# Kernel tuning notes

Measured on AMD Instinct MI355X. Metric: run time of the kernel, lower is better.

The kernel has to match this reference:

```python
import jax, jax.numpy as jnp
import numpy as np

B, S = 64, 100
N_EX, N_Q = 3000, 128
N_AT, N_IT = 1000, 1000
D_A = D_E = D_K = 128
GAMMA = 0.03


def _xavier(k, shape):
    lim = float(np.sqrt(6.0 / (shape[0] + shape[1])))
    return jax.random.uniform(k, shape, jnp.float32, -lim, lim)


def setup_inputs() -> dict:
    key = jax.random.key(0)
    ks = jax.random.split(key, 20)
    nq1 = N_Q + 1
    e_data = jax.random.randint(ks[0], (B, S), 0, N_EX, dtype=jnp.int32)
    a_data = jax.random.randint(ks[1], (B, S), 0, 2, dtype=jnp.int32)
    it_data = jax.random.randint(ks[2], (B, S), 0, N_IT, dtype=jnp.int32)
    at_data = jax.random.randint(ks[3], (B, S), 0, N_AT, dtype=jnp.int32)
    # binary Q-matrix with zeros replaced by gamma (as done in LPKT.__init__)
    q_bin = (jax.random.uniform(ks[4], (N_EX + 10, nq1)) < 0.05).astype(jnp.float32)
    q_matrix = jnp.where(q_bin > 0, 1.0, GAMMA)
    E_at = _xavier(ks[5], (N_AT + 10, D_K))
    E_it = _xavier(ks[6], (N_IT + 10, D_K))
    E_e = _xavier(ks[7], (N_EX + 10, D_E))
    h0 = _xavier(ks[8], (nq1, D_K))  # xavier-initialized initial skill state
    W1 = _xavier(ks[9], (D_A + D_E + D_K, D_K)); b1 = jnp.zeros(D_K, jnp.float32)
    W2 = _xavier(ks[10], (4 * D_K, D_K)); b2 = jnp.zeros(D_K, jnp.float32)
    W3 = _xavier(ks[11], (4 * D_K, D_K)); b3 = jnp.zeros(D_K, jnp.float32)
    W4 = _xavier(ks[12], (3 * D_K, D_K)); b4 = jnp.zeros(D_K, jnp.float32)
    W5 = _xavier(ks[13], (D_E + D_K, D_K)); b5 = jnp.zeros(D_K, jnp.float32)
    return dict(e_data=e_data, a_data=a_data, it_data=it_data, at_data=at_data,
                q_matrix=q_matrix, h0=h0, E_e=E_e, E_at=E_at, E_it=E_it,
                W1=W1, b1=b1, W2=W2, b2=b2, W3=W3, b3=b3, W4=W4, b4=b4, W5=W5, b5=b5)


def reference(e_data, a_data, it_data, at_data, q_matrix, h0, E_e, E_at, E_it,
              W1, b1, W2, b2, W3, b3, W4, b4, W5, b5):
    Bv, Sv = e_data.shape
    d_k = W2.shape[1]
    d_a = W1.shape[0] - E_e.shape[1] - d_k
    e_emb = E_e[e_data]            # (B,S,d_e)
    at_emb = E_at[at_data]         # (B,S,d_k)
    it_emb = E_it[it_data]         # (B,S,d_k)
    a_rep = jnp.broadcast_to(a_data.astype(jnp.float32)[..., None], (Bv, Sv, d_a))
    all_learning = jnp.concatenate([e_emb, at_emb, a_rep], 2) @ W1 + b1  # (B,S,d_k)
    q_all = q_matrix[e_data]       # (B,S,nq1)
    h_pre0 = jnp.broadcast_to(h0, (Bv,) + h0.shape)  # (B,nq1,d_k)
    q0 = q_all[:, 0]
    ht0 = jnp.einsum('bn,bnd->bd', q0, h_pre0) / q0.sum(1, keepdims=True)
    W4h, W4l, W4i = jnp.split(W4, 3, axis=0)

    def step(carry, x):
        learning_pre, h_pre, h_tilde_pre = carry
        q_e, q_next, it, learning, e_next = x
        feat = jnp.concatenate([learning_pre, it, learning, h_tilde_pre], 1)  # (B,4dk)
        lg = jnp.tanh(feat @ W2 + b2)
        gamma_l = jax.nn.sigmoid(feat @ W3 + b3)
        LG = gamma_l * (lg + 1.0) * 0.5                       # (B,d_k)
        LG_tilde = q_e[:, :, None] * LG[:, None, :]           # (B,nq1,d_k); dropout=eval identity
        gamma_f = jax.nn.sigmoid(jnp.einsum('bnd,df->bnf', h_pre, W4h)
                                 + (LG @ W4l + it @ W4i + b4)[:, None, :])
        h = LG_tilde + gamma_f * h_pre
        h_tilde = jnp.einsum('bn,bnd->bd', q_next, h) / q_next.sum(1, keepdims=True)
        y = jax.nn.sigmoid(jnp.concatenate([e_next, h_tilde], 1) @ W5 + b5).sum(1) / d_k
        return (learning, h, h_tilde), y

    xs = (jnp.swapaxes(q_all[:, :-1], 0, 1), jnp.swapaxes(q_all[:, 1:], 0, 1),
          jnp.swapaxes(it_emb[:, :-1], 0, 1), jnp.swapaxes(all_learning[:, :-1], 0, 1),
          jnp.swapaxes(e_emb[:, 1:], 0, 1))
    learning_pre0 = jnp.zeros((Bv, d_k), jnp.float32)
    _, ys = jax.lax.scan(step, (learning_pre0, h_pre0, ht0), xs)  # ys: (S-1,B)
    pred = jnp.zeros((Bv, Sv), jnp.float32).at[:, 1:].set(ys.T)
    return pred
```

## Files before the change

kernel.cpp:

```cpp
#include <hip/hip_runtime.h>
#include <hip/hip_fp16.h>
#include <math.h>


#define BB   64
#define SS   100
#define DK   128
#define NTH  512

#define OFF_PW1AB   0
#define OFF_PW23ABC 16384
#define OFF_PW4I    65536
#define OFF_PW5A    73728
#define OFF_PW23D   81920
#define OFF_PW4L    98304
#define OFF_AFRAG   114688
#define OFF_S1      122880
#define OFF_AL      123008
#define OFF_PRE     532608
#define OFF_HTV     2171008

typedef __attribute__((ext_vector_type(16))) float floatx16;
typedef __attribute__((ext_vector_type(8)))  short short8v;

__device__ __forceinline__ float frcp(float x) { return __builtin_amdgcn_rcpf(x); }
__device__ __forceinline__ float fsig(float x) { float t = __expf(-x); return frcp(1.0f + t); }
__device__ __forceinline__ float ftanh(float x) {
    x = fminf(20.0f, fmaxf(-20.0f, x));
    float t = __expf(-2.0f * x);
    return (1.0f - t) * frcp(1.0f + t);
}
__device__ __forceinline__ unsigned bfbits(float x) {
    unsigned u = __float_as_uint(x);
    return (u + 0x7fffu + ((u >> 16) & 1u)) >> 16;
}
__device__ __forceinline__ unsigned pack2(float a, float b) {
    return bfbits(a) | (bfbits(b) << 16);
}
__device__ __forceinline__ float blo(unsigned u) { return __uint_as_float(u << 16); }
__device__ __forceinline__ float bhi(unsigned u) { return __uint_as_float(u & 0xffff0000u); }

__device__ __forceinline__ void wg_barrier() {
    asm volatile("s_waitcnt lgkmcnt(0)" ::: "memory");
    __builtin_amdgcn_s_barrier();
    asm volatile("" ::: "memory");
}

__global__ void k0_prep(const float* __restrict__ W1, const float* __restrict__ W2,
                        const float* __restrict__ W3, const float* __restrict__ W4,
                        const float* __restrict__ W5, unsigned* __restrict__ ws) {
    int g = blockIdx.x * blockDim.x + threadIdx.x;
    if (g < 16384) {
        int s = g >> 7, d = g & 127;
        ws[OFF_PW1AB + g] = pack2(W1[(2*s)*DK + d], W1[(2*s+1)*DK + d]);
    } else if (g < 65536) {
        int i = g - 16384; int s = i >> 8, j = i & 255;
        const float* M = (j < 128) ? W2 : W3; int jj = j & 127;
        ws[g] = pack2(M[(2*s)*DK + jj], M[(2*s+1)*DK + jj]);
    } else if (g < 73728) {
        int i = g - 65536; int s = i >> 7, j = i & 127;
        ws[g] = pack2(W4[(256+2*s)*DK + j], W4[(257+2*s)*DK + j]);
    } else if (g < 81920) {
        int i = g - 73728; int s = i >> 7, j = i & 127;
        ws[g] = pack2(W5[(2*s)*DK + j], W5[(2*s+1)*DK + j]);
    } else if (g < 98304) {
        int i = g - 81920;
        int q = i & 3, ln = (i >> 2) & 63, kb = (i >> 8) & 7, cw = i >> 11;
        int k = 16*kb + 8*(ln >> 5) + 2*q;
        int j = 32*cw + (ln & 31);
        const float* M = (j < 128) ? W2 : W3; int jj = j & 127;
        ws[g] = pack2(M[(384+k)*DK + jj], M[(385+k)*DK + jj]);
    } else if (g < 106496) {
        int i = g - 98304;
        int q = i & 3, ln = (i >> 2) & 63, kb = (i >> 8) & 7, cw = i >> 11;
        int k = 16*kb + 8*(ln >> 5) + 2*q;
        int j = 32*cw + (ln & 31);
        ws[g] = pack2(W4[(128+k)*DK + j], W4[(129+k)*DK + j]);
    } else if (g < 114688) {
    } else if (g < 122880) {
        int i = g - 114688;
        int gg = i >> 11, kb = (i >> 8) & 7, ln = (i >> 2) & 63, c = i & 3;
        int m = ln & 31, hp = ln >> 5;
        int k0 = 16*kb + 8*hp + 2*c;
        ws[g] = pack2(W4[k0*DK + 32*gg + m], W4[(k0+1)*DK + 32*gg + m]);
    } else if (g < 123008) {
        int d = g - 122880;
        float z = 0.f;
        for (int k = 0; k < 128; k++) z += W1[(256+k)*DK + d];
        ws[g] = __float_as_uint(z);
    }
}

__global__ __launch_bounds__(128)
void k1_al(const int* __restrict__ e_data, const int* __restrict__ a_data,
           const int* __restrict__ at_data, const float* __restrict__ Ee,
           const float* __restrict__ Eat, const float* __restrict__ b1,
           unsigned* __restrict__ ws) {
    const int b = blockIdx.x, t0 = 4 * blockIdx.y, tid = threadIdx.x;
    __shared__ __align__(16) float s_f[4][256];
    #pragma unroll
    for (int r = 0; r < 8; r++) {
        int id = r * 128 + tid; int i = id >> 8, k = id & 255;
        int t = t0 + i; float v = 0.f;
        if (t <= 98) {
            int e  = e_data[b*SS + t];
            int at = at_data[b*SS + t];
            v = (k < 128) ? Ee[(size_t)e*DK + k] : Eat[(size_t)at*DK + (k-128)];
        }
        s_f[i][k] = v;
    }
    __syncthreads();
    float s1v = __uint_as_float(ws[OFF_S1 + tid]);
    float b1v = b1[tid];
    float z[4];
    #pragma unroll
    for (int i = 0; i < 4; i++) z[i] = 0.f;
    #pragma unroll 2
    for (int s = 0; s < 128; s++) {
        unsigned w = ws[OFF_PW1AB + s*128 + tid];
        float wl = blo(w), wh = bhi(w);
        #pragma unroll
        for (int i = 0; i < 4; i++) {
            float2 f = *(const float2*)&s_f[i][2*s];
            z[i] += f.x*wl + f.y*wh;
        }
    }
    __half* AL = (__half*)(ws + OFF_AL);
    #pragma unroll
    for (int i = 0; i < 4; i++) {
        int t = t0 + i;
        if (t <= 98) {
            float a = (float)a_data[b*SS + t];
            AL[(size_t)(b*SS + t)*DK + tid] = __float2half(z[i] + a*s1v + b1v);
        }
    }
}

__global__ __launch_bounds__(512)
void k2_pre(const int* __restrict__ e_data, const int* __restrict__ it_data,
            const float* __restrict__ Eit, const float* __restrict__ Ee,
            const float* __restrict__ b2, const float* __restrict__ b3,
            const float* __restrict__ b4, const float* __restrict__ b5,
            unsigned* __restrict__ ws) {
    const int b = blockIdx.x, t0 = 4 * blockIdx.y, tid = threadIdx.x;
    __shared__ __align__(16) float s_g[4][384];
    __shared__ __align__(16) float s_e[4][128];
    const __half* AL = (const __half*)(ws + OFF_AL);
    #pragma unroll
    for (int r = 0; r < 3; r++) {
        int id = r * 512 + tid; int i = id / 384; int k = id - 384*i;
        int t = t0 + i; float v = 0.f;
        if (t <= 98) {
            if (k < 128)      v = (t == 0) ? 0.f : (float)AL[(size_t)(b*SS + t - 1)*DK + k];
            else if (k < 256) v = Eit[(size_t)it_data[b*SS + t]*DK + (k - 128)];
            else              v = (float)AL[(size_t)(b*SS + t)*DK + (k - 256)];
        }
        s_g[i][k] = v;
    }
    {
        int id = tid; int i = id >> 7, k = id & 127;
        int t = t0 + i;
        s_e[i][k] = (t <= 98) ? Ee[(size_t)e_data[b*SS + t + 1]*DK + k] : 0.f;
    }
    __syncthreads();
    __half* PRE = (__half*)(ws + OFF_PRE);
    float z[4];
    #pragma unroll
    for (int i = 0; i < 4; i++) z[i] = 0.f;
    int col; float bb;
    if (tid < 256) {
        int j = tid;
        #pragma unroll 2
        for (int s = 0; s < 192; s++) {
            unsigned w = ws[OFF_PW23ABC + s*256 + j];
            float wl = blo(w), wh = bhi(w);
            #pragma unroll
            for (int i = 0; i < 4; i++) {
                float2 f = *(const float2*)&s_g[i][2*s];
                z[i] += f.x*wl + f.y*wh;
            }
        }
        col = j; bb = (j < 128) ? b2[j] : b3[j - 128];
    } else if (tid < 384) {
        int j = tid - 256;
        #pragma unroll 2
        for (int s = 0; s < 64; s++) {
            unsigned w = ws[OFF_PW4I + s*128 + j];
            float wl = blo(w), wh = bhi(w);
            #pragma unroll
            for (int i = 0; i < 4; i++) {
                float2 f = *(const float2*)&s_g[i][128 + 2*s];
                z[i] += f.x*wl + f.y*wh;
            }
        }
        col = 256 + j; bb = b4[j];
    } else {
        int j = tid - 384;
        #pragma unroll 2
        for (int s = 0; s < 64; s++) {
            unsigned w = ws[OFF_PW5A + s*128 + j];
            float wl = blo(w), wh = bhi(w);
            #pragma unroll
            for (int i = 0; i < 4; i++) {
                float2 f = *(const float2*)&s_e[i][2*s];
                z[i] += f.x*wl + f.y*wh;
            }
        }
        col = 384 + j; bb = b5[j];
    }
    #pragma unroll
    for (int i = 0; i < 4; i++) {
        int t = t0 + i;
        if (t <= 98) PRE[(size_t)(b*SS + t)*512 + col] = __float2half(z[i] + bb);
    }
}

__global__ __launch_bounds__(NTH, 2)
void lpkt_kernel(const int* __restrict__ e_data, const float* __restrict__ qm,
                 const float* __restrict__ h0, unsigned* __restrict__ ws)
{
    const int b    = blockIdx.x;
    const int tid  = threadIdx.x;
    const int lane = tid & 63;
    const int w    = tid >> 6;
    const int g    = w & 3;
    const int hh   = w >> 2;
    const int h5   = lane >> 5;
    const int l31  = lane & 31;
    const int hf   = w >> 2;
    const int cw3  = w & 3;

    __shared__ __align__(16) unsigned s_frag[8192];
    __shared__ __align__(16) float s_big[2 * 128 * 34];
    __shared__ __align__(16) float s_pre[2][512];
    __shared__ __align__(16) float s_LG[128];
    __shared__ __align__(16) float s_h128[128];
    __shared__ __align__(16) float s_l128[2][128];
    __shared__ __align__(16) float s_red1[256];
    __shared__ __align__(16) float s_redE[256];
    __shared__ __align__(16) unsigned s_htvb[64];
    __shared__ __align__(16) float s_q[3][160];
    __shared__ int   s_ed[100];
    __shared__ float s_scal[1];

    uint4 afru[8], pw23b[8], pw4lb[4];
    float hreg[2][16];

    #pragma unroll
    for (int kb = 0; kb < 8; kb++)
        afru[kb] = ((const uint4*)(ws + OFF_AFRAG))[g*512 + kb*64 + lane];
    #pragma unroll
    for (int kb = 0; kb < 8; kb++)
        pw23b[kb] = ((const uint4*)(ws + OFF_PW23D))[(w*8 + kb)*64 + lane];
    #pragma unroll
    for (int kbl = 0; kbl < 4; kbl++)
        pw4lb[kbl] = ((const uint4*)(ws + OFF_PW4L))[((cw3*8 + hf*4 + kbl))*64 + lane];

    const __half* PRE = (const __half*)(ws + OFF_PRE);
    __half*       HTV = (__half*)(ws + OFF_HTV);

    if (tid < 100) s_ed[tid] = e_data[b*SS + tid];
    if (tid < 160) { s_q[0][tid] = 0.f; s_q[1][tid] = 0.f; s_q[2][tid] = 0.f; }
    if (tid < 129) {
        s_q[0][tid] = qm[(size_t)e_data[b*SS + 0]*129 + tid];
        s_q[1][tid] = qm[(size_t)e_data[b*SS + 1]*129 + tid];
    }
    s_pre[0][tid] = __half2float(PRE[(size_t)(b*SS)*512 + tid]);
    float  q_pf   = (tid < 129) ? qm[(size_t)e_data[b*SS + 2]*129 + tid] : 0.f;
    __half pre_pf = PRE[(size_t)(b*SS + 1)*512 + tid];

    #pragma unroll
    for (int i = 0; i < 2; i++) {
        const int cb = 2*hh + i;
        const int n = 32*cb + l31;
        #pragma unroll
        for (int r = 0; r < 16; r++) {
            int d = 32*g + (r&3) + 8*(r>>2) + 4*h5;
            hreg[i][r] = h0[(size_t)n*DK + d];
        }
        #pragma unroll
        for (int q = 0; q < 4; q++) {
            int kb = 2*g + (q>>1);
            int lanep = l31 + ((q&1) << 5);
            int off = (((kb*4 + cb) << 10) + lanep*16 + (h5 << 3)) >> 2;
            uint2 pr = make_uint2(pack2(hreg[i][4*q],   hreg[i][4*q+1]),
                                  pack2(hreg[i][4*q+2], hreg[i][4*q+3]));
            *(uint2*)(s_frag + off) = pr;
        }
    }
    if (tid < 128) s_h128[tid] = h0[(size_t)128*DK + tid];
    __syncthreads();
    {
        if (w == 7) {
            float v = s_q[0][lane] + s_q[0][64+lane] + ((lane < 32) ? s_q[0][128+lane] : 0.f);
            #pragma unroll
            for (int m = 32; m > 0; m >>= 1) v += __shfl_xor(v, m);
            if (lane == 0) s_scal[0] = v;
        }
        float vv0[16];
        #pragma unroll
        for (int i = 0; i < 2; i++) {
            float qv = s_q[0][32*(2*hh + i) + l31];
            #pragma unroll
            for (int r = 0; r < 16; r++) {
                float p = qv * hreg[i][r];
                vv0[r] = i ? (vv0[r] + p) : p;
            }
        }
        #pragma unroll
        for (int r = 0; r < 16; r++) {
            int d = 32*g + (r&3) + 8*(r>>2) + 4*h5;
            s_big[(hh*128 + d)*34 + l31] = vv0[r];
        }
    }
    __syncthreads();
    if (tid < 128) {
        float a0 = 0.f, a1 = 0.f;
        #pragma unroll
        for (int jj = 0; jj < 16; jj++) {
            float2 x = *(const float2*)&s_big[tid*34 + 2*jj];
            float2 y = *(const float2*)&s_big[(128 + tid)*34 + 2*jj];
            a0 += x.x + x.y; a1 += y.x + y.y;
        }
        float htvv = (a0 + a1 + s_q[0][128]*s_h128[tid]) * frcp(s_scal[0]);
        float oth  = __shfl_xor(htvv, 1);
        if (!(tid & 1)) s_htvb[tid >> 1] = pack2(htvv, oth);
    }
    __syncthreads();

    for (int t = 0; t < SS - 1; t++) {
        const int pbp = t & 1;
        const float* qc = s_q[t % 3];
        const float* qn = s_q[(t + 1) % 3];

        if (t + 2 <= 99 && tid < 129) s_q[(t + 2) % 3][tid] = q_pf;
        if (t + 1 <= 98)              s_pre[1 - pbp][tid] = __half2float(pre_pf);
        if (t + 3 <= 99 && tid < 129) q_pf  = qm[(size_t)s_ed[t + 3]*129 + tid];
        if (t + 2 <= 98)              pre_pf = PRE[(size_t)(b*SS + t + 2)*512 + tid];
        if (w == 7) {
            float v = qn[lane] + qn[64 + lane] + ((lane < 32) ? qn[128 + lane] : 0.f);
            #pragma unroll
            for (int m = 32; m > 0; m >>= 1) v += __shfl_xor(v, m);
            if (lane == 0) s_scal[0] = v;
        }
        {
            floatx16 p1 = (floatx16)(0.f);
            #pragma unroll
            for (int kb = 0; kb < 8; kb++) {
                uint4 a1 = *(const uint4*)&s_htvb[kb*8 + 4*h5];
                p1 = __builtin_amdgcn_mfma_f32_32x32x16_bf16(
                        __builtin_bit_cast(short8v, a1),
                        __builtin_bit_cast(short8v, pw23b[kb]), p1, 0, 0, 0);
            }
            if (h5 == 0) s_red1[w*32 + l31] = p1[0];
        }
        floatx16 am[2];
        #pragma unroll
        for (int i = 0; i < 2; i++) {
            const int cb = 2*hh + i;
            floatx16 a = (floatx16)(0.f);
            #pragma unroll
            for (int kb = 0; kb < 8; kb++) {
                short8v bf = *(const short8v*)((const char*)s_frag +
                               (((kb*4 + cb) << 10) + lane*16));
                a = __builtin_amdgcn_mfma_f32_32x32x16_bf16(
                        __builtin_bit_cast(short8v, afru[kb]), bf, a, 0, 0, 0);
            }
            am[i] = a;
        }
        {
            float part = 0.f;
            #pragma unroll
            for (int kbl = 0; kbl < 4; kbl++) {
                const int kb = 4*hh + kbl;
                const int kb0 = 16*kb + 8*h5;
                uint4 u = afru[kb];
                part += s_h128[kb0+0]*blo(u.x) + s_h128[kb0+1]*bhi(u.x);
                part += s_h128[kb0+2]*blo(u.y) + s_h128[kb0+3]*bhi(u.y);
                part += s_h128[kb0+4]*blo(u.z) + s_h128[kb0+5]*bhi(u.z);
                part += s_h128[kb0+6]*blo(u.w) + s_h128[kb0+7]*bhi(u.w);
            }
            part += __shfl_xor(part, 32);
            if (h5 == 0) s_l128[hh][32*g + l31] = part;
        }
        wg_barrier();
        {
            const int m = 64*hf + lane;
            float z2v = s_red1[m]       + s_pre[pbp][m];
            float z3v = s_red1[128 + m] + s_pre[pbp][128 + m];
            float LGv = fsig(z3v) * (ftanh(z2v) + 1.f) * 0.5f;
            if (cw3 == 0) s_LG[m] = LGv;
            float oth = __shfl_xor(LGv, 1);
            float lo  = (lane & 1) ? oth : LGv;
            float hi  = (lane & 1) ? LGv : oth;
            int   pk  = (int)pack2(lo, hi);
            floatx16 p3 = (floatx16)(0.f);
            #pragma unroll
            for (int kbl = 0; kbl < 4; kbl++) {
                const int p0 = 8*kbl + 4*h5;
                uint4 a3;
                a3.x = (unsigned)__builtin_amdgcn_ds_bpermute(8*(p0+0), pk);
                a3.y = (unsigned)__builtin_amdgcn_ds_bpermute(8*(p0+1), pk);
                a3.z = (unsigned)__builtin_amdgcn_ds_bpermute(8*(p0+2), pk);
                a3.w = (unsigned)__builtin_amdgcn_ds_bpermute(8*(p0+3), pk);
                p3 = __builtin_amdgcn_mfma_f32_32x32x16_bf16(
                        __builtin_bit_cast(short8v, a3),
                        __builtin_bit_cast(short8v, pw4lb[kbl]), p3, 0, 0, 0);
            }
            if (h5 == 0) s_redE[hf*128 + 32*cw3 + l31] = p3[0];
        }
        wg_barrier();
        {
            float lgv[16], cvv[16], vv[16];
            const float4* LG4 = (const float4*)s_LG;
            const float4* RE4 = (const float4*)s_redE;
            const float4* PR4 = (const float4*)s_pre[pbp];
            #pragma unroll
            for (int u = 0; u < 4; u++) {
                const int idx = 8*g + 2*u + h5;
                float4 lg = LG4[idx];
                float4 c0 = RE4[idx];
                float4 c1 = RE4[32 + idx];
                float4 pv = PR4[64 + idx];
                lgv[4*u+0]=lg.x; lgv[4*u+1]=lg.y; lgv[4*u+2]=lg.z; lgv[4*u+3]=lg.w;
                cvv[4*u+0]=c0.x+c1.x+pv.x; cvv[4*u+1]=c0.y+c1.y+pv.y;
                cvv[4*u+2]=c0.z+c1.z+pv.z; cvv[4*u+3]=c0.w+c1.w+pv.w;
            }
            #pragma unroll
            for (int i = 0; i < 2; i++) {
                const int cb = 2*hh + i;
                const int n = 32*cb + l31;
                const float qcv = qc[n], qnv = qn[n];
                #pragma unroll
                for (int r = 0; r < 16; r++) {
                    float gg = fsig(am[i][r] + cvv[r]);
                    float hn = qcv*lgv[r] + gg*hreg[i][r];
                    hreg[i][r] = hn;
                    float p = qnv*hn;
                    vv[r] = i ? (vv[r] + p) : p;
                }
            }
            #pragma unroll
            for (int i = 0; i < 2; i++) {
                const int cb = 2*hh + i;
                #pragma unroll
                for (int q = 0; q < 4; q++) {
                    int kb = 2*g + (q>>1);
                    int lanep = l31 + ((q&1) << 5);
                    int off = (((kb*4 + cb) << 10) + lanep*16 + (h5 << 3)) >> 2;
                    uint2 pr = make_uint2(pack2(hreg[i][4*q],   hreg[i][4*q+1]),
                                          pack2(hreg[i][4*q+2], hreg[i][4*q+3]));
                    *(uint2*)(s_frag + off) = pr;
                }
            }
            #pragma unroll
            for (int r = 0; r < 16; r++) {
                int d = 32*g + (r&3) + 8*(r>>2) + 4*h5;
                s_big[(hh*128 + d)*34 + l31] = vv[r];
            }
            if (tid < 128) {
                float c128 = s_redE[tid] + s_redE[128 + tid] + s_pre[pbp][256 + tid];
                float gg = fsig(s_l128[0][tid] + s_l128[1][tid] + c128);
                s_h128[tid] = qc[128]*s_LG[tid] + gg*s_h128[tid];
            }
        }
        wg_barrier();
        if (tid < 128) {
            float a0 = 0.f, a1 = 0.f;
            #pragma unroll
            for (int jj = 0; jj < 16; jj++) {
                float2 x = *(const float2*)&s_big[tid*34 + 2*jj];
                float2 y = *(const float2*)&s_big[(128 + tid)*34 + 2*jj];
                a0 += x.x + x.y; a1 += y.x + y.y;
            }
            float htvv = (a0 + a1 + qn[128]*s_h128[tid]) * frcp(s_scal[0]);
            HTV[((size_t)b*(SS-1) + t)*128 + tid] = __float2half(htvv);
            float oth = __shfl_xor(htvv, 1);
            if (!(tid & 1)) s_htvb[tid >> 1] = pack2(htvv, oth);
        }
        wg_barrier();
    }
}

__global__ __launch_bounds__(128)
void k4_y(const float* __restrict__ W5, float* __restrict__ out,
          const unsigned* __restrict__ ws) {
    const int b = blockIdx.x, t = blockIdx.y, j = threadIdx.x;
    const __half* HTV = (const __half*)(ws + OFF_HTV);
    const __half* PRE = (const __half*)(ws + OFF_PRE);
    __shared__ float s_h[128];
    __shared__ float s_p[2];
    s_h[j] = __half2float(HTV[((size_t)b*(SS-1) + t)*128 + j]);
    __syncthreads();
    float z = __half2float(PRE[(size_t)(b*SS + t)*512 + 384 + j]);
    #pragma unroll 4
    for (int k = 0; k < 128; k++) z += s_h[k] * W5[(size_t)(128 + k)*DK + j];
    float v = fsig(z);
    #pragma unroll
    for (int m = 32; m > 0; m >>= 1) v += __shfl_xor(v, m);
    if ((j & 63) == 0) s_p[j >> 6] = v;
    __syncthreads();
    if (j == 0) {
        out[b*SS + t + 1] = (s_p[0] + s_p[1]) * (1.0f / 128.0f);
        if (t == 0) out[b*SS] = 0.f;
    }
}

extern "C" void kernel_launch(void* const* d_in, const int* in_sizes, int n_in,
                              void* d_out, int out_size, void* d_ws, size_t ws_size,
                              hipStream_t stream) {
    const int*   e_data  = (const int*)d_in[0];
    const int*   a_data  = (const int*)d_in[1];
    const int*   it_data = (const int*)d_in[2];
    const int*   at_data = (const int*)d_in[3];
    const float* qm  = (const float*)d_in[4];
    const float* h0  = (const float*)d_in[5];
    const float* Ee  = (const float*)d_in[6];
    const float* Eat = (const float*)d_in[7];
    const float* Eit = (const float*)d_in[8];
    const float* W1  = (const float*)d_in[9];
    const float* b1  = (const float*)d_in[10];
    const float* W2  = (const float*)d_in[11];
    const float* b2  = (const float*)d_in[12];
    const float* W3  = (const float*)d_in[13];
    const float* b3  = (const float*)d_in[14];
    const float* W4  = (const float*)d_in[15];
    const float* b4  = (const float*)d_in[16];
    const float* W5  = (const float*)d_in[17];
    const float* b5  = (const float*)d_in[18];
    float* out = (float*)d_out;
    unsigned* ws = (unsigned*)d_ws;

    k0_prep<<<dim3((123008 + 255) / 256), dim3(256), 0, stream>>>(W1, W2, W3, W4, W5, ws);
    k1_al<<<dim3(BB, 25), dim3(128), 0, stream>>>(e_data, a_data, at_data, Ee, Eat, b1, ws);
    k2_pre<<<dim3(BB, 25), dim3(512), 0, stream>>>(e_data, it_data, Eit, Ee, b2, b3, b4, b5, ws);
    lpkt_kernel<<<dim3(BB), dim3(NTH), 0, stream>>>(e_data, qm, h0, ws);
    k4_y<<<dim3(BB, SS - 1), dim3(128), 0, stream>>>(W5, out, ws);
}
```

Before: 676.7 us.

## Restructure recurrent step: move h-state MFMA before barrier, spread reduction over all waves

Moves the per-step h_pre@W4h MFMA and the node-128 dot product out of the next iteration's head into the tail of the current step, alongside the h_tilde reduction. The h_tilde reduction now uses all 512 threads with shuffles instead of 128 threads. The q-sum scalar is computed one step ahead in a double buffer. The elementwise update uses packed float2 math, exp2 and hardware v_cvt_pk_bf16_f32 for bf16 packing. This aims to shorten the serial critical path per timestep and cut VALU work, at the cost of more register pressure and reordered shared-memory hazards.

```diff
diff --git a/kernel.cpp b/kernel.cpp
--- a/kernel.cpp
+++ b/kernel.cpp
@@ -22,6 +22,7 @@
 
 typedef __attribute__((ext_vector_type(16))) float floatx16;
 typedef __attribute__((ext_vector_type(8)))  short short8v;
+typedef __attribute__((ext_vector_type(2)))  float floatx2;
 
 __device__ __forceinline__ float frcp(float x) { return __builtin_amdgcn_rcpf(x); }
 __device__ __forceinline__ float fsig(float x) { float t = __expf(-x); return frcp(1.0f + t); }
@@ -39,6 +40,12 @@
 }
 __device__ __forceinline__ float blo(unsigned u) { return __uint_as_float(u << 16); }
 __device__ __forceinline__ float bhi(unsigned u) { return __uint_as_float(u & 0xffff0000u); }
+
+__device__ __forceinline__ unsigned cvtpk(float a, float b) {
+    unsigned r;
+    asm("v_cvt_pk_bf16_f32 %0, %1, %2" : "=v"(r) : "v"(a), "v"(b));
+    return r;
+}
 
 __device__ __forceinline__ void wg_barrier() {
     asm volatile("s_waitcnt lgkmcnt(0)" ::: "memory");
@@ -241,10 +248,11 @@
     __shared__ __align__(16) unsigned s_htvb[64];
     __shared__ __align__(16) float s_q[3][160];
     __shared__ int   s_ed[100];
-    __shared__ float s_scal[1];
-
-    uint4 afru[8], pw23b[8], pw4lb[4];
-    float hreg[2][16];
+    __shared__ float s_scal[2];
+
+    uint4    afru[8], pw23b[8], pw4lb[4];
+    floatx2  hreg2[2][8];
+    floatx16 am[2];
 
     #pragma unroll
     for (int kb = 0; kb < 8; kb++)
@@ -274,87 +282,50 @@
         const int cb = 2*hh + i;
         const int n = 32*cb + l31;
         #pragma unroll
-        for (int r = 0; r < 16; r++) {
+        for (int m = 0; m < 8; m++) {
+            int r = 2*m;
             int d = 32*g + (r&3) + 8*(r>>2) + 4*h5;
-            hreg[i][r] = h0[(size_t)n*DK + d];
+            hreg2[i][m] = *(const floatx2*)&h0[(size_t)n*DK + d];
         }
         #pragma unroll
         for (int q = 0; q < 4; q++) {
             int kb = 2*g + (q>>1);
             int lanep = l31 + ((q&1) << 5);
             int off = (((kb*4 + cb) << 10) + lanep*16 + (h5 << 3)) >> 2;
-            uint2 pr = make_uint2(pack2(hreg[i][4*q],   hreg[i][4*q+1]),
-                                  pack2(hreg[i][4*q+2], hreg[i][4*q+3]));
+            uint2 pr = make_uint2(cvtpk(hreg2[i][2*q].x,   hreg2[i][2*q].y),
+                                  cvtpk(hreg2[i][2*q+1].x, hreg2[i][2*q+1].y));
             *(uint2*)(s_frag + off) = pr;
         }
     }
     if (tid < 128) s_h128[tid] = h0[(size_t)128*DK + tid];
     __syncthreads();
+
     {
         if (w == 7) {
-            float v = s_q[0][lane] + s_q[0][64+lane] + ((lane < 32) ? s_q[0][128+lane] : 0.f);
-            #pragma unroll
-            for (int m = 32; m > 0; m >>= 1) v += __shfl_xor(v, m);
-            if (lane == 0) s_scal[0] = v;
-        }
-        float vv0[16];
+            float v0 = s_q[0][lane] + s_q[0][64+lane] + ((lane < 32) ? s_q[0][128+lane] : 0.f);
+            float v1 = s_q[1][lane] + s_q[1][64+lane] + ((lane < 32) ? s_q[1][128+lane] : 0.f);
+            #pragma unroll
+            for (int m = 32; m > 0; m >>= 1) { v0 += __shfl_xor(v0, m); v1 += __shfl_xor(v1, m); }
+            if (lane == 0) { s_scal[0] = v0; s_scal[1] = v1; }
+        }
+        floatx2 vv0[8];
         #pragma unroll
         for (int i = 0; i < 2; i++) {
             float qv = s_q[0][32*(2*hh + i) + l31];
-            #pragma unroll
-            for (int r = 0; r < 16; r++) {
-                float p = qv * hreg[i][r];
-                vv0[r] = i ? (vv0[r] + p) : p;
-            }
-        }
-        #pragma unroll
-        for (int r = 0; r < 16; r++) {
+            floatx2 qv2 = {qv, qv};
+            #pragma unroll
+            for (int m = 0; m < 8; m++) {
+                if (i == 0) vv0[m] = qv2 * hreg2[i][m];
+                else        vv0[m] = vv0[m] + qv2 * hreg2[i][m];
+            }
+        }
+        #pragma unroll
+        for (int m = 0; m < 8; m++) {
+            int r = 2*m;
             int d = 32*g + (r&3) + 8*(r>>2) + 4*h5;
-            s_big[(hh*128 + d)*34 + l31] = vv0[r];
-        }
-    }
-    __syncthreads();
-    if (tid < 128) {
-        float a0 = 0.f, a1 = 0.f;
-        #pragma unroll
-        for (int jj = 0; jj < 16; jj++) {
-            float2 x = *(const float2*)&s_big[tid*34 + 2*jj];
-            float2 y = *(const float2*)&s_big[(128 + tid)*34 + 2*jj];
-            a0 += x.x + x.y; a1 += y.x + y.y;
-        }
-        float htvv = (a0 + a1 + s_q[0][128]*s_h128[tid]) * frcp(s_scal[0]);
-        float oth  = __shfl_xor(htvv, 1);
-        if (!(tid & 1)) s_htvb[tid >> 1] = pack2(htvv, oth);
-    }
-    __syncthreads();
-
-    for (int t = 0; t < SS - 1; t++) {
-        const int pbp = t & 1;
-        const float* qc = s_q[t % 3];
-        const float* qn = s_q[(t + 1) % 3];
-
-        if (t + 2 <= 99 && tid < 129) s_q[(t + 2) % 3][tid] = q_pf;
-        if (t + 1 <= 98)              s_pre[1 - pbp][tid] = __half2float(pre_pf);
-        if (t + 3 <= 99 && tid < 129) q_pf  = qm[(size_t)s_ed[t + 3]*129 + tid];
-        if (t + 2 <= 98)              pre_pf = PRE[(size_t)(b*SS + t + 2)*512 + tid];
-        if (w == 7) {
-            float v = qn[lane] + qn[64 + lane] + ((lane < 32) ? qn[128 + lane] : 0.f);
-            #pragma unroll
-            for (int m = 32; m > 0; m >>= 1) v += __shfl_xor(v, m);
-            if (lane == 0) s_scal[0] = v;
-        }
-        {
-            floatx16 p1 = (floatx16)(0.f);
-            #pragma unroll
-            for (int kb = 0; kb < 8; kb++) {
-                uint4 a1 = *(const uint4*)&s_htvb[kb*8 + 4*h5];
-                p1 = __builtin_amdgcn_mfma_f32_32x32x16_bf16(
-                        __builtin_bit_cast(short8v, a1),
-                        __builtin_bit_cast(short8v, pw23b[kb]), p1, 0, 0, 0);
-            }
-            if (h5 == 0) s_red1[w*32 + l31] = p1[0];
-        }
-        floatx16 am[2];
+            s_big[(hh*128 + d)*34 + l31]       = vv0[m].x;
+            s_big[(hh*128 + d + 1)*34 + l31]   = vv0[m].y;
+        }
         #pragma unroll
         for (int i = 0; i < 2; i++) {
             const int cb = 2*hh + i;
@@ -382,6 +353,46 @@
             }
             part += __shfl_xor(part, 32);
             if (h5 == 0) s_l128[hh][32*g + l31] = part;
+        }
+    }
+    __syncthreads();
+
+    {
+        const int row = 16*w + (lane >> 2);
+        const int qr  = lane & 3;
+        const float* basep = &s_big[(((qr >> 1) << 7) + row)*34 + ((qr & 1) << 4)];
+        floatx2 a2 = {0.f, 0.f};
+        #pragma unroll
+        for (int jj = 0; jj < 8; jj++)
+            a2 = a2 + *(const floatx2*)(basep + 2*jj);
+        float a0 = a2.x + a2.y;
+        a0 += __shfl_xor(a0, 1);
+        a0 += __shfl_xor(a0, 2);
+        float htvv = (a0 + s_q[0][128]*s_h128[row]) * frcp(s_scal[0]);
+        float oth = __shfl_down(htvv, 4);
+        if ((lane & 7) == 0) s_htvb[row >> 1] = cvtpk(htvv, oth);
+    }
+    __syncthreads();
+
+    for (int t = 0; t < SS - 1; t++) {
+        const int pbp = t & 1;
+        const float* qc = s_q[t % 3];
+        const float* qn = s_q[(t + 1) % 3];
+
+        if (t + 2 <= 99 && tid < 129) s_q[(t + 2) % 3][tid] = q_pf;
+        if (t + 1 <= 98)              s_pre[1 - pbp][tid] = __half2float(pre_pf);
+        if (t + 3 <= 99 && tid < 129) q_pf  = qm[(size_t)s_ed[t + 3]*129 + tid];
+        if (t + 2 <= 98)              pre_pf = PRE[(size_t)(b*SS + t + 2)*512 + tid];
+        {
+            floatx16 p1 = (floatx16)(0.f);
+            #pragma unroll
+            for (int kb = 0; kb < 8; kb++) {
+                uint4 a1 = *(const uint4*)&s_htvb[kb*8 + 4*h5];
+                p1 = __builtin_amdgcn_mfma_f32_32x32x16_bf16(
+                        __builtin_bit_cast(short8v, a1),
+                        __builtin_bit_cast(short8v, pw23b[kb]), p1, 0, 0, 0);
+            }
+            if (h5 == 0) s_red1[w*32 + l31] = p1[0];
         }
         wg_barrier();
         {
@@ -393,7 +404,7 @@
             float oth = __shfl_xor(LGv, 1);
             float lo  = (lane & 1) ? oth : LGv;
             float hi  = (lane & 1) ? LGv : oth;
-            int   pk  = (int)pack2(lo, hi);
+            int   pk  = (int)cvtpk(lo, hi);
             floatx16 p3 = (floatx16)(0.f);
             #pragma unroll
             for (int kbl = 0; kbl < 4; kbl++) {
@@ -411,7 +422,7 @@
         }
         wg_barrier();
         {
-            float lgv[16], cvv[16], vv[16];
+            floatx2 lg2[8], cv2[8], vv2[8];
             const float4* LG4 = (const float4*)s_LG;
             const float4* RE4 = (const float4*)s_redE;
             const float4* PR4 = (const float4*)s_pre[pbp];
@@ -422,22 +433,29 @@
                 float4 c0 = RE4[idx];
                 float4 c1 = RE4[32 + idx];
                 float4 pv = PR4[64 + idx];
-                lgv[4*u+0]=lg.x; lgv[4*u+1]=lg.y; lgv[4*u+2]=lg.z; lgv[4*u+3]=lg.w;
-                cvv[4*u+0]=c0.x+c1.x+pv.x; cvv[4*u+1]=c0.y+c1.y+pv.y;
-                cvv[4*u+2]=c0.z+c1.z+pv.z; cvv[4*u+3]=c0.w+c1.w+pv.w;
-            }
+                lg2[2*u]   = floatx2{lg.x, lg.y};
+                lg2[2*u+1] = floatx2{lg.z, lg.w};
+                cv2[2*u]   = floatx2{c0.x, c0.y} + floatx2{c1.x, c1.y} + floatx2{pv.x, pv.y};
+                cv2[2*u+1] = floatx2{c0.z, c0.w} + floatx2{c1.z, c1.w} + floatx2{pv.z, pv.w};
+            }
+            const floatx2 nl2e2 = {-1.442695041f, -1.442695041f};
             #pragma unroll
             for (int i = 0; i < 2; i++) {
                 const int cb = 2*hh + i;
                 const int n = 32*cb + l31;
                 const float qcv = qc[n], qnv = qn[n];
+                const floatx2 qc2 = {qcv, qcv};
+                const floatx2 qn2 = {qnv, qnv};
                 #pragma unroll
-                for (int r = 0; r < 16; r++) {
-                    float gg = fsig(am[i][r] + cvv[r]);
-                    float hn = qcv*lgv[r] + gg*hreg[i][r];
-                    hreg[i][r] = hn;
-                    float p = qnv*hn;
-                    vv[r] = i ? (vv[r] + p) : p;
+                for (int m = 0; m < 8; m++) {
+                    floatx2 x2 = floatx2{am[i][2*m], am[i][2*m+1]} + cv2[m];
+                    floatx2 t2 = x2 * nl2e2;
+                    floatx2 e2 = {__builtin_amdgcn_exp2f(t2.x), __builtin_amdgcn_exp2f(t2.y)};
+                    floatx2 g2 = {frcp(1.f + e2.x), frcp(1.f + e2.y)};
+                    floatx2 hn2 = qc2 * lg2[m] + g2 * hreg2[i][m];
+                    hreg2[i][m] = hn2;
+                    if (i == 0) vv2[m] = qn2 * hn2;
+                    else        vv2[m] = vv2[m] + qn2 * hn2;
                 }
             }
             #pragma unroll
@@ -448,15 +466,17 @@
                     int kb = 2*g + (q>>1);
                     int lanep = l31 + ((q&1) << 5);
                     int off = (((kb*4 + cb) << 10) + lanep*16 + (h5 << 3)) >> 2;
-                    uint2 pr = make_uint2(pack2(hreg[i][4*q],   hreg[i][4*q+1]),
-                                          pack2(hreg[i][4*q+2], hreg[i][4*q+3]));
+                    uint2 pr = make_uint2(cvtpk(hreg2[i][2*q].x,   hreg2[i][2*q].y),
+                                          cvtpk(hreg2[i][2*q+1].x, hreg2[i][2*q+1].y));
                     *(uint2*)(s_frag + off) = pr;
                 }
             }
             #pragma unroll
-            for (int r = 0; r < 16; r++) {
+            for (int m = 0; m < 8; m++) {
+                int r = 2*m;
                 int d = 32*g + (r&3) + 8*(r>>2) + 4*h5;
-                s_big[(hh*128 + d)*34 + l31] = vv[r];
+                s_big[(hh*128 + d)*34 + l31]     = vv2[m].x;
+                s_big[(hh*128 + d + 1)*34 + l31] = vv2[m].y;
             }
             if (tid < 128) {
                 float c128 = s_redE[tid] + s_redE[128 + tid] + s_pre[pbp][256 + tid];
@@ -465,18 +485,57 @@
             }
         }
         wg_barrier();
-        if (tid < 128) {
-            float a0 = 0.f, a1 = 0.f;
-            #pragma unroll
-            for (int jj = 0; jj < 16; jj++) {
-                float2 x = *(const float2*)&s_big[tid*34 + 2*jj];
-                float2 y = *(const float2*)&s_big[(128 + tid)*34 + 2*jj];
-                a0 += x.x + x.y; a1 += y.x + y.y;
-            }
-            float htvv = (a0 + a1 + qn[128]*s_h128[tid]) * frcp(s_scal[0]);
-            HTV[((size_t)b*(SS-1) + t)*128 + tid] = __float2half(htvv);
-            float oth = __shfl_xor(htvv, 1);
-            if (!(tid & 1)) s_htvb[tid >> 1] = pack2(htvv, oth);
+        #pragma unroll
+        for (int i = 0; i < 2; i++) {
+            const int cb = 2*hh + i;
+            floatx16 a = (floatx16)(0.f);
+            #pragma unroll
+            for (int kb = 0; kb < 8; kb++) {
+                short8v bf = *(const short8v*)((const char*)s_frag +
+                               (((kb*4 + cb) << 10) + lane*16));
+                a = __builtin_amdgcn_mfma_f32_32x32x16_bf16(
+                        __builtin_bit_cast(short8v, afru[kb]), bf, a, 0, 0, 0);
+            }
+            am[i] = a;
+        }
+        {
+            float part = 0.f;
+            #pragma unroll
+            for (int kbl = 0; kbl < 4; kbl++) {
+                const int kb = 4*hh + kbl;
+                const int kb0 = 16*kb + 8*h5;
+                uint4 u = afru[kb];
+                part += s_h128[kb0+0]*blo(u.x) + s_h128[kb0+1]*bhi(u.x);
+                part += s_h128[kb0+2]*blo(u.y) + s_h128[kb0+3]*bhi(u.y);
+                part += s_h128[kb0+4]*blo(u.z) + s_h128[kb0+5]*bhi(u.z);
+                part += s_h128[kb0+6]*blo(u.w) + s_h128[kb0+7]*bhi(u.w);
+            }
+            part += __shfl_xor(part, 32);
+            if (h5 == 0) s_l128[hh][32*g + l31] = part;
+        }
+        if (w == 7 && t + 2 <= 99) {
+            const float* q2 = s_q[(t + 2) % 3];
+            float v = q2[lane] + q2[64 + lane] + ((lane < 32) ? q2[128 + lane] : 0.f);
+            #pragma unroll
+            for (int m = 32; m > 0; m >>= 1) v += __shfl_xor(v, m);
+            if (lane == 0) s_scal[(t + 2) & 1] = v;
+        }
+        {
+            const int row = 16*w + (lane >> 2);
+            const int qr  = lane & 3;
+            const float* basep = &s_big[(((qr >> 1) << 7) + row)*34 + ((qr & 1) << 4)];
+            floatx2 a2 = {0.f, 0.f};
+            #pragma unroll
+            for (int jj = 0; jj < 8; jj++)
+                a2 = a2 + *(const floatx2*)(basep + 2*jj);
+            float a0 = a2.x + a2.y;
+            a0 += __shfl_xor(a0, 1);
+            a0 += __shfl_xor(a0, 2);
+            float htvv = (a0 + qn[128]*s_h128[row]) * frcp(s_scal[(t + 1) & 1]);
+            if ((lane & 3) == 0)
+                HTV[((size_t)b*(SS-1) + t)*128 + row] = __float2half(htvv);
+            float oth = __shfl_down(htvv, 4);
+            if ((lane & 7) == 0) s_htvb[row >> 1] = cvtpk(htvv, oth);
         }
         wg_barrier();
     }
```

New measurement: 644.7 us. 1.05x faster.
